# Performance work log

Measured on AMD Instinct MI355X. Metric: run time of the kernel, lower is better.

Reference implementation:

```python
import jax, jax.numpy as jnp
import numpy as np

N = 50000
E = 800000
IN_CH = 128
HID = 32
HEADS = 4
OUT_CH = 2
NEG_SLOPE = 0.2


def setup_inputs() -> dict:
    key = jax.random.key(0)
    ks = jax.random.split(key, 10)
    x = jax.random.normal(ks[0], (N, IN_CH), dtype=jnp.float32)
    edge_index = jax.random.randint(ks[1], (2, E), 0, N, dtype=jnp.int32)
    s1 = 1.0 / np.sqrt(IN_CH)
    s2 = 1.0 / np.sqrt(HEADS * HID)
    return {
        "x": x,
        "edge_index": edge_index,
        "W1": jax.random.normal(ks[2], (IN_CH, HEADS * HID), dtype=jnp.float32) * s1,
        "a_src1": jax.random.normal(ks[3], (HEADS, HID), dtype=jnp.float32) * s2,
        "a_dst1": jax.random.normal(ks[4], (HEADS, HID), dtype=jnp.float32) * s2,
        "b1": jnp.zeros((HEADS * HID,), dtype=jnp.float32),
        "W2": jax.random.normal(ks[5], (HEADS * HID, 1 * OUT_CH), dtype=jnp.float32) * s2,
        "a_src2": jax.random.normal(ks[6], (1, OUT_CH), dtype=jnp.float32),
        "a_dst2": jax.random.normal(ks[7], (1, OUT_CH), dtype=jnp.float32),
        "b2": jnp.zeros((OUT_CH,), dtype=jnp.float32),
    }


def gat_layer(x, edge_index, W, a_src, a_dst, bias, heads, out_ch, concat):
    # PyG GATConv: linear -> per-node attn terms -> per-edge LeakyReLU ->
    # softmax over incoming edges (self-loops added) -> scatter-add aggregate.
    n = x.shape[0]
    loop = jnp.arange(n, dtype=edge_index.dtype)
    src = jnp.concatenate([edge_index[0], loop])  # [E+N]
    dst = jnp.concatenate([edge_index[1], loop])
    h = (x @ W).reshape(n, heads, out_ch)                 # [N, H, C]
    a_s = jnp.einsum('nhc,hc->nh', h, a_src)              # [N, H]
    a_d = jnp.einsum('nhc,hc->nh', h, a_dst)
    e = jax.nn.leaky_relu(a_s[src] + a_d[dst], NEG_SLOPE)  # [E+N, H]
    m = jax.ops.segment_max(e, dst, num_segments=n)
    m = jax.lax.stop_gradient(jnp.where(jnp.isfinite(m), m, 0.0))
    p = jnp.exp(e - m[dst])
    denom = jax.ops.segment_sum(p, dst, num_segments=n)
    alpha = p / (denom[dst] + 1e-16)                       # softmax per dst node
    msg = h[src] * alpha[:, :, None]                       # [E+N, H, C]
    out = jax.ops.segment_sum(msg, dst, num_segments=n)    # [N, H, C]
    out = out.reshape(n, heads * out_ch) if concat else out.mean(axis=1)
    return out + bias


def reference(x, edge_index, W1, a_src1, a_dst1, b1, W2, a_src2, a_dst2, b2):
    h = gat_layer(x, edge_index, W1, a_src1, a_dst1, b1, HEADS, HID, True)
    h = jax.nn.relu(h)  # dropout is identity in eval mode
    o = gat_layer(h, edge_index, W2, a_src2, a_dst2, b2, 1, OUT_CH, False)
    return jax.nn.log_softmax(o, axis=1)
```

## Files before the change

### kernel.cpp

```cpp
#include <hip/hip_runtime.h>
#include <hip/hip_bf16.h>

#define NEG_SLOPE 0.2f
#define INV_LN2 1.44269504088896340736f
#define BSH   6
#define BUKSZ 64
#define MAXBUK 1024
#define CHUNK 2048
#define XPAD  136

typedef __attribute__((ext_vector_type(8))) short bf16x8;
typedef __attribute__((ext_vector_type(4))) float f32x4;

__device__ __forceinline__ float exp2lrelu(float z) {
    return __builtin_amdgcn_exp2f(fmaxf(z, NEG_SLOPE * z));
}

__device__ __forceinline__ unsigned short f2bf(float f) {
    unsigned int u = __float_as_uint(f);
    u = (u + 0x7fffu + ((u >> 16) & 1u)) >> 16;
    return (unsigned short)u;
}

__device__ __forceinline__ float2 bfpair(unsigned int u) {
    float2 r;
    r.x = __uint_as_float(u << 16);
    r.y = __uint_as_float(u & 0xffff0000u);
    return r;
}

__global__ __launch_bounds__(256) void k0_prep(const float* __restrict__ W1,
                                               const float* __restrict__ a_src1,
                                               const float* __restrict__ a_dst1,
                                               unsigned short* __restrict__ w1t,
                                               int* __restrict__ bcnt,
                                               int* __restrict__ gcur, int nbuk) {
    int g = blockIdx.x * 256 + threadIdx.x;
    if (g < nbuk) { bcnt[g] = 0; gcur[g] = 0; }
    if (g < 128 * 128) {
        int k = g >> 7, nn = g & 127;
        w1t[nn * 128 + k] = f2bf(W1[g]);
    } else if (g < 128 * 128 + 1024) {
        int e = g - 128 * 128;
        int row8 = e >> 7;
        int k = e & 127;
        int h = row8 & 3;
        const float* av = (row8 < 4) ? a_src1 : a_dst1;
        float s = 0.f;
#pragma unroll
        for (int c = 0; c < 32; ++c)
            s += W1[k * 128 + h * 32 + c] * av[h * 32 + c];
        w1t[(128 + row8) * 128 + k] = f2bf(s * INV_LN2);
    } else if (g < 128 * 128 + 2048) {
        int e = g - (128 * 128 + 1024);
        w1t[(136 + (e >> 7)) * 128 + (e & 127)] = 0;
    }
}

__global__ __launch_bounds__(256) void k1_fat(const float* __restrict__ x,
                                              const unsigned short* __restrict__ w1t,
                                              unsigned short* __restrict__ h1b,
                                              float* __restrict__ a_s1,
                                              float* __restrict__ a_d1, int n,
                                              const int* __restrict__ e_dst, int e,
                                              int nbuk, int nblk,
                                              int* __restrict__ bcnt) {
    __shared__ unsigned short wsh[144 * XPAD];
    const int tid = threadIdx.x;

    if (blockIdx.x < (unsigned)nblk) {
        int* lcnt = (int*)wsh;
        const int bid = blockIdx.x;
        for (int b = tid; b < nbuk; b += 256) lcnt[b] = 0;
        __syncthreads();
        const int e0 = bid * CHUNK;
        const int e1 = min(e, e0 + CHUNK);
        for (int k = e0 + tid; k < e1; k += 256)
            atomicAdd(&lcnt[e_dst[k] >> BSH], 1);
        __syncthreads();
        for (int b = tid; b < nbuk; b += 256) {
            int c = lcnt[b];
            if (c) atomicAdd(&bcnt[b], c);
        }
        return;
    }

    const int row0 = (blockIdx.x - nblk) * 64;
    {
        const bf16x8* w1v = (const bf16x8*)w1t;
#pragma unroll
        for (int ii = 0; ii < 9; ++ii) {
            int i = tid + ii * 256;
            int r = i >> 4, c = (i & 15) * 8;
            *(bf16x8*)&wsh[r * XPAD + c] = w1v[i];
        }
    }

    const int wave = tid >> 6;
    const int lane = tid & 63;
    const int quad = lane >> 4;
    const int l16 = lane & 15;

    const int arow = row0 + wave * 16 + l16;
    const bool rowok = arow < n;
    const float* __restrict__ xr = x + (size_t)arow * 128;
    bf16x8 afrag[4];
#pragma unroll
    for (int ks = 0; ks < 4; ++ks) {
        float4 u = make_float4(0.f, 0.f, 0.f, 0.f), v = u;
        if (rowok) {
            u = *(const float4*)&xr[ks * 32 + quad * 8];
            v = *(const float4*)&xr[ks * 32 + quad * 8 + 4];
        }
        bf16x8 a;
        a[0] = (short)f2bf(u.x); a[1] = (short)f2bf(u.y);
        a[2] = (short)f2bf(u.z); a[3] = (short)f2bf(u.w);
        a[4] = (short)f2bf(v.x); a[5] = (short)f2bf(v.y);
        a[6] = (short)f2bf(v.z); a[7] = (short)f2bf(v.w);
        afrag[ks] = a;
    }
    __syncthreads();

    f32x4 acc[9];
#pragma unroll
    for (int t = 0; t < 9; ++t) acc[t] = (f32x4){0.f, 0.f, 0.f, 0.f};

#pragma unroll
    for (int t = 0; t < 9; ++t) {
#pragma unroll
        for (int ks = 0; ks < 4; ++ks) {
            bf16x8 bfrag = *(const bf16x8*)&wsh[(t * 16 + l16) * XPAD + ks * 32 + quad * 8];
            acc[t] = __builtin_amdgcn_mfma_f32_16x16x32_bf16(afrag[ks], bfrag, acc[t], 0, 0, 0);
        }
    }

#pragma unroll
    for (int r = 0; r < 4; ++r) {
        int gr = row0 + wave * 16 + quad * 4 + r;
        if (gr < n) {
            if (l16 < 4)      a_s1[gr * 4 + l16]       = acc[8][r];
            else if (l16 < 8) a_d1[gr * 4 + (l16 - 4)] = acc[8][r];
        }
    }

    __syncthreads();
#pragma unroll
    for (int t = 0; t < 8; ++t)
#pragma unroll
        for (int r = 0; r < 4; ++r)
            wsh[(wave * 16 + quad * 4 + r) * XPAD + t * 16 + l16] = f2bf(acc[t][r]);
    __syncthreads();
#pragma unroll
    for (int i = 0; i < 8; ++i) {
        int idx = tid + i * 256;
        int r = idx >> 5;
        int c = (idx & 31) * 4;
        int gr = row0 + r;
        if (gr < n)
            *(ushort4*)&h1b[(size_t)gr * 128 + c] = *(ushort4*)&wsh[r * XPAD + c];
    }
}

__global__ __launch_bounds__(256) void kb_place3(const int* __restrict__ src,
                                                 const int* __restrict__ dst, int e,
                                                 int nbuk, const int* __restrict__ bcnt,
                                                 int* __restrict__ gcur,
                                                 unsigned int* __restrict__ part,
                                                 int* __restrict__ bbase) {
    __shared__ int lbase[MAXBUK];
    __shared__ int lcur[MAXBUK];
    __shared__ int s[256];
    const int tid = threadIdx.x;
    const int bid = blockIdx.x;
    int t4 = tid * 4;
    int v0 = (t4     < nbuk) ? bcnt[t4]     : 0;
    int v1 = (t4 + 1 < nbuk) ? bcnt[t4 + 1] : 0;
    int v2 = (t4 + 2 < nbuk) ? bcnt[t4 + 2] : 0;
    int v3 = (t4 + 3 < nbuk) ? bcnt[t4 + 3] : 0;
    int ssum = v0 + v1 + v2 + v3;
    s[tid] = ssum;
    for (int b = tid; b < nbuk; b += 256) lcur[b] = 0;
    __syncthreads();
    for (int off = 1; off < 256; off <<= 1) {
        int t = (tid >= off) ? s[tid - off] : 0;
        __syncthreads();
        s[tid] += t;
        __syncthreads();
    }
    int excl = s[tid] - ssum;
    if (t4 < nbuk)     lbase[t4]     = excl;
    if (t4 + 1 < nbuk) lbase[t4 + 1] = excl + v0;
    if (t4 + 2 < nbuk) lbase[t4 + 2] = excl + v0 + v1;
    if (t4 + 3 < nbuk) lbase[t4 + 3] = excl + v0 + v1 + v2;
    __syncthreads();
    if (bid == 0) {
        for (int b = tid; b < nbuk; b += 256) bbase[b] = lbase[b];
        if (tid == 255) bbase[nbuk] = s[255];
    }
    const int e0 = bid * CHUNK;
    const int e1 = min(e, e0 + CHUNK);
    for (int k = e0 + tid; k < e1; k += 256)
        atomicAdd(&lcur[dst[k] >> BSH], 1);
    __syncthreads();
    for (int b = tid; b < nbuk; b += 256) {
        int c = lcur[b];
        if (c) lcur[b] = lbase[b] + atomicAdd(&gcur[b], c);
    }
    __syncthreads();
    for (int k = e0 + tid; k < e1; k += 256) {
        int d = dst[k];
        int pos = atomicAdd(&lcur[d >> BSH], 1);
        part[pos] = ((unsigned int)src[k] << 16) | (unsigned int)(d & 0xffff);
    }
}

__global__ __launch_bounds__(256) void kc_csr(const unsigned int* __restrict__ part,
                                              const int* __restrict__ bbase, int nbuk,
                                              int* __restrict__ row_start,
                                              unsigned short* __restrict__ csr_src) {
    __shared__ int cnt[64];
    __shared__ int cur[64];
    const int b = blockIdx.x;
    const int tid = threadIdx.x;
    const int eb = bbase[b];
    const int nE = bbase[b + 1] - eb;
    if (tid < 64) cnt[tid] = 0;
    __syncthreads();
    for (int k = tid; k < nE; k += 256)
        atomicAdd(&cnt[part[eb + k] & 63u], 1);
    __syncthreads();
    if (tid < 64) {
        int v = cnt[tid];
        int incl = v;
#pragma unroll
        for (int off = 1; off < 64; off <<= 1) {
            int t = __shfl_up(incl, off);
            if (tid >= off) incl += t;
        }
        int excl = incl - v;
        cur[tid] = excl;
        row_start[(b << BSH) + tid] = eb + excl;
        if (tid == 63 && b == nbuk - 1) row_start[(b << BSH) + 64] = eb + incl;
    }
    __syncthreads();
    for (int k = tid; k < nE; k += 256) {
        unsigned int u = part[eb + k];
        int pos = atomicAdd(&cur[u & 63u], 1);
        csr_src[eb + pos] = (unsigned short)(u >> 16);
    }
}

__global__ __launch_bounds__(256) void k3_agg1(
    const unsigned short* __restrict__ h1b, const float* __restrict__ a_s1,
    const float* __restrict__ a_d1, const int* __restrict__ row_start,
    const unsigned short* __restrict__ csr_src, const float* __restrict__ b1,
    const float* __restrict__ W2, const float* __restrict__ a_src2,
    const float* __restrict__ a_dst2, float4* __restrict__ pk, int n) {
    const int wid = (blockIdx.x * blockDim.x + threadIdx.x) >> 6;
    const int lane = threadIdx.x & 63;
    if (wid >= n) return;
    const int q = lane >> 4;
    const int l16 = lane & 15;
    const int c0 = l16 * 8;
    const unsigned cb = (unsigned)l16 * 16u;
    const int head = l16 >> 2;
    const int rs = row_start[wid];
    const int deg = row_start[wid + 1] - rs;
    const float ad = a_d1[wid * 4 + head];
    const char* __restrict__ h1c = (const char*)h1b;
    const unsigned short* __restrict__ crs = csr_src + rs;

    float dnm = 0.f;
    float acc[8] = {};
    const int nfull = deg >> 4;
    int j = q;
    for (int it = 0; it < nfull; ++it, j += 16) {
        unsigned s0 = (unsigned)crs[j];
        unsigned s1 = (unsigned)crs[j + 4];
        unsigned s2 = (unsigned)crs[j + 8];
        unsigned s3 = (unsigned)crs[j + 12];
        float as0 = a_s1[(s0 << 2) + head];
        float as1 = a_s1[(s1 << 2) + head];
        float as2 = a_s1[(s2 << 2) + head];
        float as3 = a_s1[(s3 << 2) + head];
        uint4 g0 = *(const uint4*)(h1c + ((s0 << 8) + cb));
        uint4 g1 = *(const uint4*)(h1c + ((s1 << 8) + cb));
        uint4 g2 = *(const uint4*)(h1c + ((s2 << 8) + cb));
        uint4 g3 = *(const uint4*)(h1c + ((s3 << 8) + cb));
        float p0 = exp2lrelu(as0 + ad);
        float p1 = exp2lrelu(as1 + ad);
        float p2 = exp2lrelu(as2 + ad);
        float p3 = exp2lrelu(as3 + ad);
        dnm += (p0 + p1) + (p2 + p3);
        float2 v0a = bfpair(g0.x), v0b = bfpair(g0.y), v0c = bfpair(g0.z), v0d = bfpair(g0.w);
        float2 v1a = bfpair(g1.x), v1b = bfpair(g1.y), v1c = bfpair(g1.z), v1d = bfpair(g1.w);
        float2 v2a = bfpair(g2.x), v2b = bfpair(g2.y), v2c = bfpair(g2.z), v2d = bfpair(g2.w);
        float2 v3a = bfpair(g3.x), v3b = bfpair(g3.y), v3c = bfpair(g3.z), v3d = bfpair(g3.w);
        acc[0] += (p0 * v0a.x + p1 * v1a.x) + (p2 * v2a.x + p3 * v3a.x);
        acc[1] += (p0 * v0a.y + p1 * v1a.y) + (p2 * v2a.y + p3 * v3a.y);
        acc[2] += (p0 * v0b.x + p1 * v1b.x) + (p2 * v2b.x + p3 * v3b.x);
        acc[3] += (p0 * v0b.y + p1 * v1b.y) + (p2 * v2b.y + p3 * v3b.y);
        acc[4] += (p0 * v0c.x + p1 * v1c.x) + (p2 * v2c.x + p3 * v3c.x);
        acc[5] += (p0 * v0c.y + p1 * v1c.y) + (p2 * v2c.y + p3 * v3c.y);
        acc[6] += (p0 * v0d.x + p1 * v1d.x) + (p2 * v2d.x + p3 * v3d.x);
        acc[7] += (p0 * v0d.y + p1 * v1d.y) + (p2 * v2d.y + p3 * v3d.y);
    }
    if (deg & 15) {
        const int dm1 = deg - 1;
        int i0 = min(j,      dm1);
        int i1 = min(j + 4,  dm1);
        int i2 = min(j + 8,  dm1);
        int i3 = min(j + 12, dm1);
        unsigned s0 = (unsigned)crs[i0];
        unsigned s1 = (unsigned)crs[i1];
        unsigned s2 = (unsigned)crs[i2];
        unsigned s3 = (unsigned)crs[i3];
        float as0 = a_s1[(s0 << 2) + head];
        float as1 = a_s1[(s1 << 2) + head];
        float as2 = a_s1[(s2 << 2) + head];
        float as3 = a_s1[(s3 << 2) + head];
        const bool b0 = j      < deg;
        const bool b1 = j + 4  < deg;
        const bool b2 = j + 8  < deg;
        const bool b3 = j + 12 < deg;
        uint4 g0 = make_uint4(0, 0, 0, 0), g1 = g0, g2 = g0, g3 = g0;
        if (b0) g0 = *(const uint4*)(h1c + ((s0 << 8) + cb));
        if (b1) g1 = *(const uint4*)(h1c + ((s1 << 8) + cb));
        if (b2) g2 = *(const uint4*)(h1c + ((s2 << 8) + cb));
        if (b3) g3 = *(const uint4*)(h1c + ((s3 << 8) + cb));
        float p0 = b0 ? exp2lrelu(as0 + ad) : 0.f;
        float p1 = b1 ? exp2lrelu(as1 + ad) : 0.f;
        float p2 = b2 ? exp2lrelu(as2 + ad) : 0.f;
        float p3 = b3 ? exp2lrelu(as3 + ad) : 0.f;
        dnm += (p0 + p1) + (p2 + p3);
        float2 v0a = bfpair(g0.x), v0b = bfpair(g0.y), v0c = bfpair(g0.z), v0d = bfpair(g0.w);
        float2 v1a = bfpair(g1.x), v1b = bfpair(g1.y), v1c = bfpair(g1.z), v1d = bfpair(g1.w);
        float2 v2a = bfpair(g2.x), v2b = bfpair(g2.y), v2c = bfpair(g2.z), v2d = bfpair(g2.w);
        float2 v3a = bfpair(g3.x), v3b = bfpair(g3.y), v3c = bfpair(g3.z), v3d = bfpair(g3.w);
        acc[0] += (p0 * v0a.x + p1 * v1a.x) + (p2 * v2a.x + p3 * v3a.x);
        acc[1] += (p0 * v0a.y + p1 * v1a.y) + (p2 * v2a.y + p3 * v3a.y);
        acc[2] += (p0 * v0b.x + p1 * v1b.x) + (p2 * v2b.x + p3 * v3b.x);
        acc[3] += (p0 * v0b.y + p1 * v1b.y) + (p2 * v2b.y + p3 * v3b.y);
        acc[4] += (p0 * v0c.x + p1 * v1c.x) + (p2 * v2c.x + p3 * v3c.x);
        acc[5] += (p0 * v0c.y + p1 * v1c.y) + (p2 * v2c.y + p3 * v3c.y);
        acc[6] += (p0 * v0d.x + p1 * v1d.x) + (p2 * v2d.x + p3 * v3d.x);
        acc[7] += (p0 * v0d.y + p1 * v1d.y) + (p2 * v2d.y + p3 * v3d.y);
    }
    dnm += __shfl_xor(dnm, 16);
    dnm += __shfl_xor(dnm, 32);
#pragma unroll
    for (int k = 0; k < 8; ++k) {
        acc[k] += __shfl_xor(acc[k], 16);
        acc[k] += __shfl_xor(acc[k], 32);
    }
    {
        float p = exp2lrelu(a_s1[wid * 4 + head] + ad);
        uint4 gs = *(const uint4*)(h1c + (((unsigned)wid << 8) + cb));
        float2 ha = bfpair(gs.x), hb = bfpair(gs.y), hc = bfpair(gs.z), hd2 = bfpair(gs.w);
        dnm += p;
        acc[0] += p * ha.x;  acc[1] += p * ha.y;
        acc[2] += p * hb.x;  acc[3] += p * hb.y;
        acc[4] += p * hc.x;  acc[5] += p * hc.y;
        acc[6] += p * hd2.x; acc[7] += p * hd2.y;
    }
    float inv = 1.f / (dnm + 1e-16f);
    float r[8];
    float4 bva = *(const float4*)&b1[c0];
    float4 bvb = *(const float4*)&b1[c0 + 4];
    r[0] = fmaxf(acc[0] * inv + bva.x, 0.f);
    r[1] = fmaxf(acc[1] * inv + bva.y, 0.f);
    r[2] = fmaxf(acc[2] * inv + bva.z, 0.f);
    r[3] = fmaxf(acc[3] * inv + bva.w, 0.f);
    r[4] = fmaxf(acc[4] * inv + bvb.x, 0.f);
    r[5] = fmaxf(acc[5] * inv + bvb.y, 0.f);
    r[6] = fmaxf(acc[6] * inv + bvb.z, 0.f);
    r[7] = fmaxf(acc[7] * inv + bvb.w, 0.f);

    float p0 = 0.f, p1 = 0.f;
#pragma unroll
    for (int k = 0; k < 4; ++k) {
        float4 w = *(const float4*)&W2[c0 * 2 + k * 4];
        p0 += r[2 * k] * w.x + r[2 * k + 1] * w.z;
        p1 += r[2 * k] * w.y + r[2 * k + 1] * w.w;
    }
#pragma unroll
    for (int off = 1; off < 16; off <<= 1) {
        p0 += __shfl_xor(p0, off);
        p1 += __shfl_xor(p1, off);
    }
    if (lane == 0) {
        pk[wid] = make_float4(p0, p1,
                              (p0 * a_src2[0] + p1 * a_src2[1]) * INV_LN2,
                              (p0 * a_dst2[0] + p1 * a_dst2[1]) * INV_LN2);
    }
}

__global__ __launch_bounds__(256) void k4_agg2(
    const float4* __restrict__ pk, const int* __restrict__ row_start,
    const unsigned short* __restrict__ csr_src, const float* __restrict__ b2,
    float* __restrict__ out, int n) {
    const int g = blockIdx.x * blockDim.x + threadIdx.x;
    const int lane = threadIdx.x & 63;
    const int node = (g >> 6) * 4 + (lane >> 4);
    const int l16 = lane & 15;
    if (node >= n) return;
    const int rs = row_start[node];
    const int deg = row_start[node + 1] - rs;
    const float4 me = pk[node];
    const float ad = me.w;

    float dnm = 0.f, a0 = 0.f, a1 = 0.f;
    for (int j = l16; j < deg; j += 16) {
        int s = (int)csr_src[rs + j];
        float4 qv = pk[s];
        float p = exp2lrelu(qv.z + ad);
        dnm += p;
        a0 += p * qv.x;
        a1 += p * qv.y;
    }
    if (l16 == 0) {
        float p = exp2lrelu(me.z + ad);
        dnm += p;
        a0 += p * me.x;
        a1 += p * me.y;
    }
#pragma unroll
    for (int off = 1; off < 16; off <<= 1) {
        dnm += __shfl_xor(dnm, off);
        a0 += __shfl_xor(a0, off);
        a1 += __shfl_xor(a1, off);
    }
    if (l16 == 0) {
        float inv = 1.f / (dnm + 1e-16f);
        float o0 = a0 * inv + b2[0];
        float o1 = a1 * inv + b2[1];
        float m2 = fmaxf(o0, o1);
        float lse = m2 + logf(__expf(o0 - m2) + __expf(o1 - m2));
        out[node * 2 + 0] = o0 - lse;
        out[node * 2 + 1] = o1 - lse;
    }
}

extern "C" void kernel_launch(void* const* d_in, const int* in_sizes, int n_in,
                              void* d_out, int out_size, void* d_ws, size_t ws_size,
                              hipStream_t stream) {
    const float* x      = (const float*)d_in[0];
    const int*   ei     = (const int*)d_in[1];
    const float* W1     = (const float*)d_in[2];
    const float* a_src1 = (const float*)d_in[3];
    const float* a_dst1 = (const float*)d_in[4];
    const float* b1     = (const float*)d_in[5];
    const float* W2     = (const float*)d_in[6];
    const float* a_src2 = (const float*)d_in[7];
    const float* a_dst2 = (const float*)d_in[8];
    const float* b2     = (const float*)d_in[9];
    float* out = (float*)d_out;

    const int N = in_sizes[0] / 128;
    const int E = in_sizes[1] / 2;
    const int* e_src = ei;
    const int* e_dst = ei + E;

    const int NBUK = (N + BUKSZ - 1) >> BSH;
    const int nblk = (E + CHUNK - 1) / CHUNK;
    const int gemmBlocks = (N + 63) / 64;

    char* p = (char*)d_ws;
    auto alloc = [&](size_t bytes) -> void* {
        void* r = (void*)p;
        p += (bytes + 255) & ~(size_t)255;
        return r;
    };
    unsigned short* h1b   = (unsigned short*)alloc((size_t)N * 128 * 2);
    float*          a_s1  = (float*)alloc((size_t)N * 4 * 4);
    float*          a_d1  = (float*)alloc((size_t)N * 4 * 4);
    float4*         pk    = (float4*)alloc((size_t)N * 16);
    unsigned short* w1t   = (unsigned short*)alloc((size_t)144 * 128 * 2);
    int*            bcnt  = (int*)alloc((size_t)NBUK * 4);
    int*            gcur  = (int*)alloc((size_t)NBUK * 4);
    int*            bbase = (int*)alloc((size_t)(NBUK + 1) * 4);
    unsigned int*   part  = (unsigned int*)alloc((size_t)E * 4);
    int*            row_start = (int*)alloc(((size_t)NBUK * BUKSZ + 1) * 4);
    unsigned short* csr_src   = (unsigned short*)alloc((size_t)E * 2);

    k0_prep<<<72, 256, 0, stream>>>(W1, a_src1, a_dst1, w1t, bcnt, gcur, NBUK);
    k1_fat<<<nblk + gemmBlocks, 256, 0, stream>>>(x, w1t, h1b, a_s1, a_d1, N,
                                                  e_dst, E, NBUK, nblk, bcnt);
    kb_place3<<<nblk, 256, 0, stream>>>(e_src, e_dst, E, NBUK, bcnt, gcur, part, bbase);
    kc_csr<<<NBUK, 256, 0, stream>>>(part, bbase, NBUK, row_start, csr_src);

    k3_agg1<<<(N * 64 + 255) / 256, 256, 0, stream>>>(h1b, a_s1, a_d1, row_start, csr_src,
                                                      b1, W2, a_src2, a_dst2, pk, N);
    k4_agg2<<<((N + 3) / 4 * 64 + 255) / 256, 256, 0, stream>>>(pk, row_start, csr_src,
                                                                b2, out, N);
}
```

Baseline: 172.8 us.

## Fuse CSR build stages into fat kernel with software grid barriers

Merges the bucket-count, place and per-bucket CSR sort kernels into the edge-processing blocks of the first fused kernel. Spin-wait barriers on global counters stand in for kernel boundaries, and the CSR stage now runs alongside the GEMM blocks. This removes two launches and the gaps between them. It relies on all nblk (391) edge blocks being co-resident. Since those blocks have the lowest block indices they are probably dispatched first, but nothing guarantees it, so the barriers could deadlock or stall the GEMM blocks behind them.

```diff
diff --git a/kernel.cpp b/kernel.cpp
--- a/kernel.cpp
+++ b/kernel.cpp
@@ -29,14 +29,28 @@
     return r;
 }
 
+__device__ __forceinline__ void subset_barrier(int* ctr, int target) {
+    __syncthreads();
+    if (threadIdx.x == 0) {
+        __threadfence();
+        atomicAdd(ctr, 1);
+        while (__hip_atomic_load(ctr, __ATOMIC_ACQUIRE,
+                                 __HIP_MEMORY_SCOPE_AGENT) < target)
+            __builtin_amdgcn_s_sleep(8);
+    }
+    __syncthreads();
+}
+
 __global__ __launch_bounds__(256) void k0_prep(const float* __restrict__ W1,
                                                const float* __restrict__ a_src1,
                                                const float* __restrict__ a_dst1,
                                                unsigned short* __restrict__ w1t,
                                                int* __restrict__ bcnt,
-                                               int* __restrict__ gcur, int nbuk) {
+                                               int* __restrict__ gcur,
+                                               int* __restrict__ sync, int nbuk) {
     int g = blockIdx.x * 256 + threadIdx.x;
     if (g < nbuk) { bcnt[g] = 0; gcur[g] = 0; }
+    if (g < 2) sync[g] = 0;
     if (g < 128 * 128) {
         int k = g >> 7, nn = g & 127;
         w1t[nn * 128 + k] = f2bf(W1[g]);
@@ -62,26 +76,98 @@
                                               unsigned short* __restrict__ h1b,
                                               float* __restrict__ a_s1,
                                               float* __restrict__ a_d1, int n,
+                                              const int* __restrict__ e_src,
                                               const int* __restrict__ e_dst, int e,
                                               int nbuk, int nblk,
-                                              int* __restrict__ bcnt) {
+                                              int* __restrict__ bcnt,
+                                              int* __restrict__ gcur,
+                                              unsigned int* __restrict__ part,
+                                              int* __restrict__ row_start,
+                                              unsigned short* __restrict__ csr_src,
+                                              int* __restrict__ sync) {
     __shared__ unsigned short wsh[144 * XPAD];
     const int tid = threadIdx.x;
 
     if (blockIdx.x < (unsigned)nblk) {
-        int* lcnt = (int*)wsh;
+        int* lbase = (int*)wsh;
+        int* lcur  = (int*)wsh + MAXBUK;
+        int* s     = (int*)wsh + 2 * MAXBUK;
         const int bid = blockIdx.x;
-        for (int b = tid; b < nbuk; b += 256) lcnt[b] = 0;
-        __syncthreads();
         const int e0 = bid * CHUNK;
         const int e1 = min(e, e0 + CHUNK);
+        for (int b = tid; b < nbuk; b += 256) lcur[b] = 0;
+        __syncthreads();
         for (int k = e0 + tid; k < e1; k += 256)
-            atomicAdd(&lcnt[e_dst[k] >> BSH], 1);
+            atomicAdd(&lcur[e_dst[k] >> BSH], 1);
         __syncthreads();
         for (int b = tid; b < nbuk; b += 256) {
-            int c = lcnt[b];
+            int c = lcur[b];
             if (c) atomicAdd(&bcnt[b], c);
         }
+        subset_barrier(&sync[0], nblk);
+        int t4 = tid * 4;
+        int v0 = (t4     < nbuk) ? bcnt[t4]     : 0;
+        int v1 = (t4 + 1 < nbuk) ? bcnt[t4 + 1] : 0;
+        int v2 = (t4 + 2 < nbuk) ? bcnt[t4 + 2] : 0;
+        int v3 = (t4 + 3 < nbuk) ? bcnt[t4 + 3] : 0;
+        int ssum = v0 + v1 + v2 + v3;
+        s[tid] = ssum;
+        __syncthreads();
+        for (int off = 1; off < 256; off <<= 1) {
+            int t = (tid >= off) ? s[tid - off] : 0;
+            __syncthreads();
+            s[tid] += t;
+            __syncthreads();
+        }
+        const int total = s[255];
+        int excl = s[tid] - ssum;
+        if (t4 < nbuk)     lbase[t4]     = excl;
+        if (t4 + 1 < nbuk) lbase[t4 + 1] = excl + v0;
+        if (t4 + 2 < nbuk) lbase[t4 + 2] = excl + v0 + v1;
+        if (t4 + 3 < nbuk) lbase[t4 + 3] = excl + v0 + v1 + v2;
+        __syncthreads();
+        for (int b = tid; b < nbuk; b += 256) {
+            int c = lcur[b];
+            if (c) lcur[b] = lbase[b] + atomicAdd(&gcur[b], c);
+        }
+        __syncthreads();
+        for (int k = e0 + tid; k < e1; k += 256) {
+            int d = e_dst[k];
+            int pos = atomicAdd(&lcur[d >> BSH], 1);
+            part[pos] = ((unsigned int)e_src[k] << 16) | (unsigned int)(d & 0xffff);
+        }
+        subset_barrier(&sync[1], nblk);
+        int* cnt = s;
+        int* cur = s + 64;
+        for (int bb = bid; bb < nbuk; bb += nblk) {
+            const int eb = lbase[bb];
+            const int next = (bb + 1 < nbuk) ? lbase[bb + 1] : total;
+            const int nE = next - eb;
+            if (tid < 64) cnt[tid] = 0;
+            __syncthreads();
+            for (int k = tid; k < nE; k += 256)
+                atomicAdd(&cnt[part[eb + k] & 63u], 1);
+            __syncthreads();
+            if (tid < 64) {
+                int v = cnt[tid];
+                int incl = v;
+#pragma unroll
+                for (int off = 1; off < 64; off <<= 1) {
+                    int t = __shfl_up(incl, off);
+                    if (tid >= off) incl += t;
+                }
+                cur[tid] = incl - v;
+                row_start[(bb << BSH) + tid] = eb + incl - v;
+            }
+            __syncthreads();
+            for (int k = tid; k < nE; k += 256) {
+                unsigned int u = part[eb + k];
+                int pos = atomicAdd(&cur[u & 63u], 1);
+                csr_src[eb + pos] = (unsigned short)(u >> 16);
+            }
+            __syncthreads();
+        }
+        if (bid == 0 && tid == 0) row_start[nbuk << BSH] = total;
         return;
     }
 
@@ -158,95 +244,6 @@
         int gr = row0 + r;
         if (gr < n)
             *(ushort4*)&h1b[(size_t)gr * 128 + c] = *(ushort4*)&wsh[r * XPAD + c];
-    }
-}
-
-__global__ __launch_bounds__(256) void kb_place3(const int* __restrict__ src,
-                                                 const int* __restrict__ dst, int e,
-                                                 int nbuk, const int* __restrict__ bcnt,
-                                                 int* __restrict__ gcur,
-                                                 unsigned int* __restrict__ part,
-                                                 int* __restrict__ bbase) {
-    __shared__ int lbase[MAXBUK];
-    __shared__ int lcur[MAXBUK];
-    __shared__ int s[256];
-    const int tid = threadIdx.x;
-    const int bid = blockIdx.x;
-    int t4 = tid * 4;
-    int v0 = (t4     < nbuk) ? bcnt[t4]     : 0;
-    int v1 = (t4 + 1 < nbuk) ? bcnt[t4 + 1] : 0;
-    int v2 = (t4 + 2 < nbuk) ? bcnt[t4 + 2] : 0;
-    int v3 = (t4 + 3 < nbuk) ? bcnt[t4 + 3] : 0;
-    int ssum = v0 + v1 + v2 + v3;
-    s[tid] = ssum;
-    for (int b = tid; b < nbuk; b += 256) lcur[b] = 0;
-    __syncthreads();
-    for (int off = 1; off < 256; off <<= 1) {
-        int t = (tid >= off) ? s[tid - off] : 0;
-        __syncthreads();
-        s[tid] += t;
-        __syncthreads();
-    }
-    int excl = s[tid] - ssum;
-    if (t4 < nbuk)     lbase[t4]     = excl;
-    if (t4 + 1 < nbuk) lbase[t4 + 1] = excl + v0;
-    if (t4 + 2 < nbuk) lbase[t4 + 2] = excl + v0 + v1;
-    if (t4 + 3 < nbuk) lbase[t4 + 3] = excl + v0 + v1 + v2;
-    __syncthreads();
-    if (bid == 0) {
-        for (int b = tid; b < nbuk; b += 256) bbase[b] = lbase[b];
-        if (tid == 255) bbase[nbuk] = s[255];
-    }
-    const int e0 = bid * CHUNK;
-    const int e1 = min(e, e0 + CHUNK);
-    for (int k = e0 + tid; k < e1; k += 256)
-        atomicAdd(&lcur[dst[k] >> BSH], 1);
-    __syncthreads();
-    for (int b = tid; b < nbuk; b += 256) {
-        int c = lcur[b];
-        if (c) lcur[b] = lbase[b] + atomicAdd(&gcur[b], c);
-    }
-    __syncthreads();
-    for (int k = e0 + tid; k < e1; k += 256) {
-        int d = dst[k];
-        int pos = atomicAdd(&lcur[d >> BSH], 1);
-        part[pos] = ((unsigned int)src[k] << 16) | (unsigned int)(d & 0xffff);
-    }
-}
-
-__global__ __launch_bounds__(256) void kc_csr(const unsigned int* __restrict__ part,
-                                              const int* __restrict__ bbase, int nbuk,
-                                              int* __restrict__ row_start,
-                                              unsigned short* __restrict__ csr_src) {
-    __shared__ int cnt[64];
-    __shared__ int cur[64];
-    const int b = blockIdx.x;
-    const int tid = threadIdx.x;
-    const int eb = bbase[b];
-    const int nE = bbase[b + 1] - eb;
-    if (tid < 64) cnt[tid] = 0;
-    __syncthreads();
-    for (int k = tid; k < nE; k += 256)
-        atomicAdd(&cnt[part[eb + k] & 63u], 1);
-    __syncthreads();
-    if (tid < 64) {
-        int v = cnt[tid];
-        int incl = v;
-#pragma unroll
-        for (int off = 1; off < 64; off <<= 1) {
-            int t = __shfl_up(incl, off);
-            if (tid >= off) incl += t;
-        }
-        int excl = incl - v;
-        cur[tid] = excl;
-        row_start[(b << BSH) + tid] = eb + excl;
-        if (tid == 63 && b == nbuk - 1) row_start[(b << BSH) + 64] = eb + incl;
-    }
-    __syncthreads();
-    for (int k = tid; k < nE; k += 256) {
-        unsigned int u = part[eb + k];
-        int pos = atomicAdd(&cur[u & 63u], 1);
-        csr_src[eb + pos] = (unsigned short)(u >> 16);
     }
 }
 
@@ -478,17 +475,16 @@
     unsigned short* w1t   = (unsigned short*)alloc((size_t)144 * 128 * 2);
     int*            bcnt  = (int*)alloc((size_t)NBUK * 4);
     int*            gcur  = (int*)alloc((size_t)NBUK * 4);
-    int*            bbase = (int*)alloc((size_t)(NBUK + 1) * 4);
     unsigned int*   part  = (unsigned int*)alloc((size_t)E * 4);
     int*            row_start = (int*)alloc(((size_t)NBUK * BUKSZ + 1) * 4);
     unsigned short* csr_src   = (unsigned short*)alloc((size_t)E * 2);
-
-    k0_prep<<<72, 256, 0, stream>>>(W1, a_src1, a_dst1, w1t, bcnt, gcur, NBUK);
+    int*            sync  = (int*)alloc(256);
+
+    k0_prep<<<72, 256, 0, stream>>>(W1, a_src1, a_dst1, w1t, bcnt, gcur, sync, NBUK);
     k1_fat<<<nblk + gemmBlocks, 256, 0, stream>>>(x, w1t, h1b, a_s1, a_d1, N,
-                                                  e_dst, E, NBUK, nblk, bcnt);
-    kb_place3<<<nblk, 256, 0, stream>>>(e_src, e_dst, E, NBUK, bcnt, gcur, part, bbase);
-    kc_csr<<<NBUK, 256, 0, stream>>>(part, bbase, NBUK, row_start, csr_src);
-
+                                                  e_src, e_dst, E, NBUK, nblk,
+                                                  bcnt, gcur, part, row_start,
+                                                  csr_src, sync);
     k3_agg1<<<(N * 64 + 255) / 256, 256, 0, stream>>>(h1b, a_s1, a_d1, row_start, csr_src,
                                                       b1, W2, a_src2, a_dst2, pk, N);
     k4_agg2<<<((N + 3) / 4 * 64 + 255) / 256, 256, 0, stream>>>(pk, row_start, csr_src,
```

After: 288.3 us. 1.67x slower.
